# Performance work log

Measured on AMD Instinct MI355X. Metric: run time of the kernel, lower is better.

## Reference

```python
import jax, jax.numpy as jnp
import numpy as np

B, N, C = 4, 2048, 768
H = 12
HD = C // H  # 64


def setup_inputs() -> dict:
    key = jax.random.key(0)
    ks = jax.random.split(key, 6)
    s = 0.02
    return {
        "x": jax.random.normal(ks[0], (B, N, C), dtype=jnp.float32),
        "w_qkv": jax.random.normal(ks[1], (C, 3 * C), dtype=jnp.float32) * s,
        "b_qkv": jax.random.normal(ks[2], (3 * C,), dtype=jnp.float32) * s,
        "w_proj": jax.random.normal(ks[3], (C, C), dtype=jnp.float32) * s,
        "b_proj": jax.random.normal(ks[4], (C,), dtype=jnp.float32) * s,
        "key_log_bias": jax.random.normal(ks[5], (B, N), dtype=jnp.float32),
    }


def reference(x, w_qkv, b_qkv, w_proj, b_proj, key_log_bias):
    b, n, c = x.shape
    scale = 1.0 / float(HD) ** 0.5
    qkv = x @ w_qkv + b_qkv                      # [B, N, 3C]
    qkv = qkv.reshape(b, n, 3, H, HD).transpose(2, 0, 3, 1, 4)  # [3, B, H, N, HD]
    q, k, v = qkv[0], qkv[1], qkv[2]
    logits = jnp.einsum('bhqd,bhkd->bhqk', q, k) * scale        # [B, H, N, N]
    logits = logits + key_log_bias[:, None, None, :]            # key-side bias
    attn = jax.nn.softmax(logits, axis=-1)
    out = jnp.einsum('bhqk,bhkd->bhqd', attn, v)                # [B, H, N, HD]
    out = out.transpose(0, 2, 1, 3).reshape(b, n, c)            # [B, N, C]
    return out @ w_proj + b_proj
```

## Files before the change

### kernel.cpp

```cpp
#include <hip/hip_runtime.h>


typedef short short8 __attribute__((ext_vector_type(8)));
typedef float f32x4 __attribute__((ext_vector_type(4)));
typedef unsigned int u32x4 __attribute__((ext_vector_type(4)));

#define GLB_AS(p) ((const __attribute__((address_space(1))) void*)(p))
#define LDS_AS(p) ((__attribute__((address_space(3))) void*)(p))

__device__ __forceinline__ void gload_lds16(const void* g, void* l) {
  __builtin_amdgcn_global_load_lds(GLB_AS(g), LDS_AS(l), 16, 0, 0);
}

__device__ __forceinline__ f32x4 mfma16(short8 a, short8 b, f32x4 c) {
  return __builtin_amdgcn_mfma_f32_16x16x32_bf16(a, b, c, 0, 0, 0);
}

__device__ __forceinline__ unsigned short f2bf(float f) {
  union { float f; unsigned u; } v; v.f = f;
  unsigned r = v.u + 0x7fffu + ((v.u >> 16) & 1u);
  return (unsigned short)(r >> 16);
}

__device__ __forceinline__ unsigned cvt_pk_bf16(float a, float b) {
  unsigned r;
  asm("v_cvt_pk_bf16_f32 %0, %1, %2" : "=v"(r) : "v"(a), "v"(b));
  return r;
}

#define LOG2E 1.44269504088896340736f

__device__ __forceinline__ int kappa1(int m) {
  return ((m >> 4) & 1) * 32 + ((m >> 2) & 3) * 8 + ((m >> 5) & 1) * 4 + (m & 3);
}


__global__ __launch_bounds__(256) void cvt_f32_bf16(const float* __restrict__ in,
                                                    unsigned short* __restrict__ out,
                                                    int n8) {
  int i = blockIdx.x * 256 + threadIdx.x;
  if (i >= n8) return;
  const float4* p = (const float4*)in + 2 * (size_t)i;
  float4 a = p[0], c = p[1];
  short8 r;
  r[0] = (short)f2bf(a.x); r[1] = (short)f2bf(a.y); r[2] = (short)f2bf(a.z); r[3] = (short)f2bf(a.w);
  r[4] = (short)f2bf(c.x); r[5] = (short)f2bf(c.y); r[6] = (short)f2bf(c.z); r[7] = (short)f2bf(c.w);
  ((short8*)out)[i] = r;
}

__global__ __launch_bounds__(256) void scale_bias(const float* __restrict__ in,
                                                  float* __restrict__ out, int n) {
  int i = blockIdx.x * 256 + threadIdx.x;
  if (i >= n) return;
  int m = i & 63;
  out[i] = in[(i & ~63) + kappa1(m)] * LOG2E;
}

__global__ __launch_bounds__(256) void tr_cvt_f32_bf16(const float* __restrict__ src,
                                                       unsigned short* __restrict__ dst,
                                                       int R, int C) {
  __shared__ float t[32][33];
  int tx = threadIdx.x & 31, ty = threadIdx.x >> 5;
  int c0 = blockIdx.x * 32, r0 = blockIdx.y * 32;
#pragma unroll
  for (int i = 0; i < 32; i += 8)
    t[ty + i][tx] = src[(size_t)(r0 + ty + i) * C + c0 + tx];
  __syncthreads();
#pragma unroll
  for (int i = 0; i < 32; i += 8)
    dst[(size_t)(c0 + ty + i) * R + r0 + tx] = f2bf(t[tx][ty + i]);
}

__global__ __launch_bounds__(256) void tr_bf16_head(const unsigned short* __restrict__ src,
                                                    unsigned short* __restrict__ dst) {
  __shared__ unsigned short t[32][33];
  int tx = threadIdx.x & 31, ty = threadIdx.x >> 5;
  size_t hb = (size_t)blockIdx.z * (2048 * 64);
  int c0 = blockIdx.x * 32, r0 = blockIdx.y * 32;
#pragma unroll
  for (int i = 0; i < 32; i += 8)
    t[ty + i][tx] = src[hb + (size_t)(r0 + ty + i) * 64 + c0 + tx];
  __syncthreads();
#pragma unroll
  for (int i = 0; i < 32; i += 8)
    dst[hb + (size_t)(c0 + ty + i) * 2048 + r0 + tx] = t[tx][ty + i];
}

template <int EPI>
__global__ __launch_bounds__(256, 2) void gemm_bt(
    const unsigned short* __restrict__ A, const unsigned short* __restrict__ Bt,
    const float* __restrict__ bias, float* __restrict__ outf,
    unsigned short* __restrict__ qo, unsigned short* __restrict__ ko,
    unsigned short* __restrict__ vo, int K) {
  __shared__ __align__(16) unsigned short As[128 * 64];
  __shared__ __align__(16) unsigned short Bs[128 * 64];
  const int tid = threadIdx.x;
  const int lane = tid & 63, wid = tid >> 6;
  const int lr = lane & 15, lg = lane >> 4;
  const int bm = blockIdx.x, bn = blockIdx.y;
  const int wr = (wid >> 1) * 64, wc = (wid & 1) * 64;

  const unsigned short* ap[4];
  const unsigned short* bp[4];
  unsigned loff[4];
#pragma unroll
  for (int i = 0; i < 4; ++i) {
    int c = wid * 4 + i;
    int r = c * 8 + (lane >> 3);
    int gs = (lane & 7) ^ (r & 7);
    ap[i] = A + (size_t)(bm * 128 + r) * K + gs * 8;
    bp[i] = Bt + (size_t)(bn * 128 + r) * K + gs * 8;
    loff[i] = (unsigned)c * 1024;
  }

  f32x4 acc[4][4] = {};
  const int nt = K >> 6;
  for (int t = 0; t < nt; ++t) {
#pragma unroll
    for (int i = 0; i < 4; ++i) {
      gload_lds16(ap[i], (char*)As + loff[i]);
      gload_lds16(bp[i], (char*)Bs + loff[i]);
      ap[i] += 64;
      bp[i] += 64;
    }
    __syncthreads();
#pragma unroll
    for (int kkk = 0; kkk < 2; ++kkk) {
      short8 af[4], bf[4];
#pragma unroll
      for (int mf = 0; mf < 4; ++mf) {
        int r = wr + mf * 16 + lr;
        int g = kkk * 4 + lg;
        af[mf] = *(const short8*)((const char*)As + r * 128 + ((g ^ (r & 7)) << 4));
      }
#pragma unroll
      for (int nf = 0; nf < 4; ++nf) {
        int r = wc + nf * 16 + lr;
        int g = kkk * 4 + lg;
        bf[nf] = *(const short8*)((const char*)Bs + r * 128 + ((g ^ (r & 7)) << 4));
      }
#pragma unroll
      for (int mf = 0; mf < 4; ++mf)
#pragma unroll
        for (int nf = 0; nf < 4; ++nf)
          acc[mf][nf] = mfma16(af[mf], bf[nf], acc[mf][nf]);
    }
    __syncthreads();
  }

  const int colbase = bn * 128 + wc;
  float bv[4];
#pragma unroll
  for (int nf = 0; nf < 4; ++nf) bv[nf] = bias[colbase + nf * 16 + lr];

  if constexpr (EPI == 0) {
#pragma unroll
    for (int nf = 0; nf < 4; ++nf) {
      int col = colbase + nf * 16 + lr;
      int which = col / 768;
      int rem = col - which * 768;
      int h = rem >> 6, d = rem & 63;
#pragma unroll
      for (int mf = 0; mf < 4; ++mf) {
#pragma unroll
        for (int j = 0; j < 4; ++j) {
          int row = bm * 128 + wr + mf * 16 + lg * 4 + j;
          int bb = row >> 11, nn = row & 2047;
          float v = acc[mf][nf][j] + bv[nf];
          size_t off = (((size_t)bb * 12 + h) * 2048 + nn) * 64 + d;
          if (which == 0)
            qo[off] = f2bf(v * (0.125f * LOG2E));
          else if (which == 1)
            ko[off] = f2bf(v);
          else
            vo[off] = f2bf(v);
        }
      }
    }
  } else {
#pragma unroll
    for (int mf = 0; mf < 4; ++mf) {
#pragma unroll
      for (int j = 0; j < 4; ++j) {
        int row = bm * 128 + wr + mf * 16 + lg * 4 + j;
#pragma unroll
        for (int nf = 0; nf < 4; ++nf) {
          int col = colbase + nf * 16 + lr;
          outf[(size_t)row * 768 + col] = acc[mf][nf][j] + bv[nf];
        }
      }
    }
  }
}

__global__ __launch_bounds__(256, 3) void attn_fused(
    const unsigned short* __restrict__ Q, const unsigned short* __restrict__ Kx,
    const unsigned short* __restrict__ Vt, const float* __restrict__ klb,
    unsigned short* __restrict__ Ao) {
  __shared__ __align__(16) unsigned short Ks[64 * 64];
  __shared__ __align__(16) unsigned short Vs[64 * 64];
  const int tid = threadIdx.x, lane = tid & 63, wid = tid >> 6;
  const int lr = lane & 15, lg = lane >> 4;
  const int qb = blockIdx.x, bh = blockIdx.y;
  const int b = bh / 12, h = bh - b * 12;
  const size_t hoff = (size_t)bh * (2048 * 64);
  const unsigned short* Qh = Q + hoff;
  const unsigned short* Kh = Kx + hoff;
  const unsigned short* Vh = Vt + hoff;
  const float* kb = klb + b * 2048;

  short8 qf[2][2];
#pragma unroll
  for (int mf = 0; mf < 2; ++mf)
#pragma unroll
    for (int kkk = 0; kkk < 2; ++kkk) {
      int qr = qb * 128 + wid * 32 + mf * 16 + lr;
      qf[mf][kkk] = *(const short8*)(Qh + (size_t)qr * 64 + kkk * 32 + lg * 8);
    }

  const int c0 = wid * 2, c1 = wid * 2 + 1;
  const int r0s = c0 * 8 + (lane >> 3), r1s = c1 * 8 + (lane >> 3);
  const int g0 = (lane & 7) ^ (r0s & 7), g1 = (lane & 7) ^ (r1s & 7);
  const int k1r0 = kappa1(r0s), k1r1 = kappa1(r1s);

  f32x4 o[2][4] = {};
  f32x4 ol[2] = {};

  short8 ones;
#pragma unroll
  for (int e = 0; e < 8; ++e) ones[e] = (short)0x3F80;

  for (int t = 0; t < 32; ++t) {
    const int kt0 = t * 64;
    gload_lds16(Kh + (size_t)(kt0 + k1r0) * 64 + g0 * 8, (char*)Ks + c0 * 1024);
    gload_lds16(Kh + (size_t)(kt0 + k1r1) * 64 + g1 * 8, (char*)Ks + c1 * 1024);
    gload_lds16(Vh + (size_t)r0s * 2048 + kt0 + g0 * 8, (char*)Vs + c0 * 1024);
    gload_lds16(Vh + (size_t)r1s * 2048 + kt0 + g1 * 8, (char*)Vs + c1 * 1024);
    __syncthreads();

    f32x4 bias4[4];
#pragma unroll
    for (int nf = 0; nf < 4; ++nf)
      bias4[nf] = *(const f32x4*)(kb + kt0 + nf * 16 + lg * 4);

    f32x4 s[4][2] = {};
#pragma unroll
    for (int kkk = 0; kkk < 2; ++kkk) {
      short8 kf[4];
#pragma unroll
      for (int nf = 0; nf < 4; ++nf) {
        int r = nf * 16 + lr, g = kkk * 4 + lg;
        kf[nf] = *(const short8*)((const char*)Ks + r * 128 + ((g ^ (r & 7)) << 4));
      }
#pragma unroll
      for (int nf = 0; nf < 4; ++nf)
#pragma unroll
        for (int mf = 0; mf < 2; ++mf)
          s[nf][mf] = mfma16(kf[nf], qf[mf][kkk], s[nf][mf]);
    }

#pragma unroll
    for (int nf = 0; nf < 4; ++nf)
#pragma unroll
      for (int mf = 0; mf < 2; ++mf)
#pragma unroll
        for (int j = 0; j < 4; ++j)
          s[nf][mf][j] = __builtin_exp2f(s[nf][mf][j] + bias4[nf][j]);

    short8 pa[2][2];
#pragma unroll
    for (int mf = 0; mf < 2; ++mf)
#pragma unroll
      for (int kkk = 0; kkk < 2; ++kkk) {
        u32x4 w;
        w[0] = cvt_pk_bf16(s[kkk][mf][0], s[kkk][mf][1]);
        w[1] = cvt_pk_bf16(s[kkk][mf][2], s[kkk][mf][3]);
        w[2] = cvt_pk_bf16(s[kkk + 2][mf][0], s[kkk + 2][mf][1]);
        w[3] = cvt_pk_bf16(s[kkk + 2][mf][2], s[kkk + 2][mf][3]);
        pa[mf][kkk] = __builtin_bit_cast(short8, w);
      }

#pragma unroll
    for (int kkk = 0; kkk < 2; ++kkk) {
      short8 vf[4];
#pragma unroll
      for (int nf = 0; nf < 4; ++nf) {
        int r = nf * 16 + lr, g = kkk * 4 + lg;
        vf[nf] = *(const short8*)((const char*)Vs + r * 128 + ((g ^ (r & 7)) << 4));
      }
#pragma unroll
      for (int mf = 0; mf < 2; ++mf) {
        ol[mf] = mfma16(pa[mf][kkk], ones, ol[mf]);
#pragma unroll
        for (int nf = 0; nf < 4; ++nf)
          o[mf][nf] = mfma16(pa[mf][kkk], vf[nf], o[mf][nf]);
      }
    }
    __syncthreads();
  }

#pragma unroll
  for (int mf = 0; mf < 2; ++mf)
#pragma unroll
    for (int j = 0; j < 4; ++j) {
      float inv = 1.f / ol[mf][j];
      int qr = qb * 128 + wid * 32 + mf * 16 + lg * 4 + j;
#pragma unroll
      for (int nf = 0; nf < 4; ++nf) {
        int d = nf * 16 + lr;
        Ao[((size_t)b * 2048 + qr) * 768 + h * 64 + d] = f2bf(o[mf][nf][j] * inv);
      }
    }
}


extern "C" void kernel_launch(void* const* d_in, const int* in_sizes, int n_in,
                              void* d_out, int out_size, void* d_ws, size_t ws_size,
                              hipStream_t stream) {
  (void)in_sizes; (void)n_in; (void)out_size; (void)ws_size;
  const float* x = (const float*)d_in[0];
  const float* wqkv = (const float*)d_in[1];
  const float* bqkv = (const float*)d_in[2];
  const float* wproj = (const float*)d_in[3];
  const float* bproj = (const float*)d_in[4];
  const float* klb = (const float*)d_in[5];
  float* out = (float*)d_out;
  char* ws = (char*)d_ws;

  const size_t SZ = (size_t)8192 * 768 * 2;
  unsigned short* xb = (unsigned short*)(ws);
  unsigned short* wqkvT = (unsigned short*)(ws + SZ);
  unsigned short* wprojT = (unsigned short*)(ws + SZ + 3538944);
  unsigned short* qbuf = (unsigned short*)(ws + SZ + 3538944 + 1179648);
  unsigned short* kbuf = (unsigned short*)(ws + SZ + 3538944 + 1179648 + SZ);
  unsigned short* vbuf = (unsigned short*)(ws + SZ + 3538944 + 1179648 + 2 * SZ);
  unsigned short* vtbuf = (unsigned short*)(ws + SZ + 3538944 + 1179648 + 3 * SZ);
  float* klbs = (float*)(ws + SZ + 3538944 + 1179648 + 4 * SZ);
  unsigned short* aob = xb;

  cvt_f32_bf16<<<dim3(3072), dim3(256), 0, stream>>>(x, xb, 786432);
  scale_bias<<<dim3(32), dim3(256), 0, stream>>>(klb, klbs, 8192);
  tr_cvt_f32_bf16<<<dim3(72, 24), dim3(256), 0, stream>>>(wqkv, wqkvT, 768, 2304);
  tr_cvt_f32_bf16<<<dim3(24, 24), dim3(256), 0, stream>>>(wproj, wprojT, 768, 768);
  gemm_bt<0><<<dim3(64, 18), dim3(256), 0, stream>>>(xb, wqkvT, bqkv, nullptr,
                                                     qbuf, kbuf, vbuf, 768);
  tr_bf16_head<<<dim3(2, 64, 48), dim3(256), 0, stream>>>(vbuf, vtbuf);
  attn_fused<<<dim3(16, 48), dim3(256), 0, stream>>>(qbuf, kbuf, vtbuf, klbs, aob);
  gemm_bt<1><<<dim3(64, 6), dim3(256), 0, stream>>>(aob, wprojT, bproj, out,
                                                    nullptr, nullptr, nullptr, 768);
}
```

Measured before the change: 166.2 us.

## Fold exp(key bias) into V and row-sum weights; double-buffer K/V tiles

Result: faster. 158.5 us (-4.6%).

```diff
diff --git a/kernel.cpp b/kernel.cpp
--- a/kernel.cpp
+++ b/kernel.cpp
@@ -20,6 +20,11 @@
   union { float f; unsigned u; } v; v.f = f;
   unsigned r = v.u + 0x7fffu + ((v.u >> 16) & 1u);
   return (unsigned short)(r >> 16);
+}
+
+__device__ __forceinline__ float bf2f(unsigned short u) {
+  union { unsigned u; float f; } v; v.u = ((unsigned)u) << 16;
+  return v.f;
 }
 
 __device__ __forceinline__ unsigned cvt_pk_bf16(float a, float b) {
@@ -48,12 +53,10 @@
   ((short8*)out)[i] = r;
 }
 
-__global__ __launch_bounds__(256) void scale_bias(const float* __restrict__ in,
-                                                  float* __restrict__ out, int n) {
+__global__ __launch_bounds__(256) void exp_bias(const float* __restrict__ in,
+                                                unsigned short* __restrict__ out, int n) {
   int i = blockIdx.x * 256 + threadIdx.x;
-  if (i >= n) return;
-  int m = i & 63;
-  out[i] = in[(i & ~63) + kappa1(m)] * LOG2E;
+  if (i < n) out[i] = f2bf(__builtin_exp2f(in[i] * LOG2E));
 }
 
 __global__ __launch_bounds__(256) void tr_cvt_f32_bf16(const float* __restrict__ src,
@@ -72,18 +75,21 @@
 }
 
 __global__ __launch_bounds__(256) void tr_bf16_head(const unsigned short* __restrict__ src,
+                                                    const unsigned short* __restrict__ ebb,
                                                     unsigned short* __restrict__ dst) {
   __shared__ unsigned short t[32][33];
   int tx = threadIdx.x & 31, ty = threadIdx.x >> 5;
   size_t hb = (size_t)blockIdx.z * (2048 * 64);
+  int b = blockIdx.z / 12;
   int c0 = blockIdx.x * 32, r0 = blockIdx.y * 32;
 #pragma unroll
   for (int i = 0; i < 32; i += 8)
     t[ty + i][tx] = src[hb + (size_t)(r0 + ty + i) * 64 + c0 + tx];
   __syncthreads();
+  float eb = bf2f(ebb[b * 2048 + r0 + tx]);
 #pragma unroll
   for (int i = 0; i < 32; i += 8)
-    dst[hb + (size_t)(c0 + ty + i) * 2048 + r0 + tx] = t[tx][ty + i];
+    dst[hb + (size_t)(c0 + ty + i) * 2048 + r0 + tx] = f2bf(bf2f(t[tx][ty + i]) * eb);
 }
 
 template <int EPI>
@@ -195,10 +201,10 @@
 
 __global__ __launch_bounds__(256, 3) void attn_fused(
     const unsigned short* __restrict__ Q, const unsigned short* __restrict__ Kx,
-    const unsigned short* __restrict__ Vt, const float* __restrict__ klb,
+    const unsigned short* __restrict__ Vt, const unsigned short* __restrict__ ebb,
     unsigned short* __restrict__ Ao) {
-  __shared__ __align__(16) unsigned short Ks[64 * 64];
-  __shared__ __align__(16) unsigned short Vs[64 * 64];
+  __shared__ __align__(16) unsigned short Ks[2][64 * 64];
+  __shared__ __align__(16) unsigned short Vs[2][64 * 64];
   const int tid = threadIdx.x, lane = tid & 63, wid = tid >> 6;
   const int lr = lane & 15, lg = lane >> 4;
   const int qb = blockIdx.x, bh = blockIdx.y;
@@ -207,7 +213,7 @@
   const unsigned short* Qh = Q + hoff;
   const unsigned short* Kh = Kx + hoff;
   const unsigned short* Vh = Vt + hoff;
-  const float* kb = klb + b * 2048;
+  const unsigned short* ebh = ebb + b * 2048;
 
   short8 qf[2][2];
 #pragma unroll
@@ -226,22 +232,28 @@
   f32x4 o[2][4] = {};
   f32x4 ol[2] = {};
 
-  short8 ones;
-#pragma unroll
-  for (int e = 0; e < 8; ++e) ones[e] = (short)0x3F80;
+#define STAGE(buf, t)                                                                  \
+  do {                                                                                 \
+    const int kt0_ = (t) * 64;                                                         \
+    gload_lds16(Kh + (size_t)(kt0_ + k1r0) * 64 + g0 * 8, (char*)Ks[buf] + c0 * 1024); \
+    gload_lds16(Kh + (size_t)(kt0_ + k1r1) * 64 + g1 * 8, (char*)Ks[buf] + c1 * 1024); \
+    gload_lds16(Vh + (size_t)r0s * 2048 + kt0_ + g0 * 8, (char*)Vs[buf] + c0 * 1024);  \
+    gload_lds16(Vh + (size_t)r1s * 2048 + kt0_ + g1 * 8, (char*)Vs[buf] + c1 * 1024);  \
+  } while (0)
+
+  STAGE(0, 0);
+  int cur = 0;
 
   for (int t = 0; t < 32; ++t) {
+    __syncthreads();
+    if (t + 1 < 32) STAGE(cur ^ 1, t + 1);
+
     const int kt0 = t * 64;
-    gload_lds16(Kh + (size_t)(kt0 + k1r0) * 64 + g0 * 8, (char*)Ks + c0 * 1024);
-    gload_lds16(Kh + (size_t)(kt0 + k1r1) * 64 + g1 * 8, (char*)Ks + c1 * 1024);
-    gload_lds16(Vh + (size_t)r0s * 2048 + kt0 + g0 * 8, (char*)Vs + c0 * 1024);
-    gload_lds16(Vh + (size_t)r1s * 2048 + kt0 + g1 * 8, (char*)Vs + c1 * 1024);
-    __syncthreads();
-
-    f32x4 bias4[4];
-#pragma unroll
-    for (int nf = 0; nf < 4; ++nf)
-      bias4[nf] = *(const f32x4*)(kb + kt0 + nf * 16 + lg * 4);
+
+    short8 ebf[2];
+#pragma unroll
+    for (int kkk = 0; kkk < 2; ++kkk)
+      ebf[kkk] = *(const short8*)(ebh + kt0 + kkk * 32 + lg * 8);
 
     f32x4 s[4][2] = {};
 #pragma unroll
@@ -250,7 +262,7 @@
 #pragma unroll
       for (int nf = 0; nf < 4; ++nf) {
         int r = nf * 16 + lr, g = kkk * 4 + lg;
-        kf[nf] = *(const short8*)((const char*)Ks + r * 128 + ((g ^ (r & 7)) << 4));
+        kf[nf] = *(const short8*)((const char*)Ks[cur] + r * 128 + ((g ^ (r & 7)) << 4));
       }
 #pragma unroll
       for (int nf = 0; nf < 4; ++nf)
@@ -265,7 +277,7 @@
       for (int mf = 0; mf < 2; ++mf)
 #pragma unroll
         for (int j = 0; j < 4; ++j)
-          s[nf][mf][j] = __builtin_exp2f(s[nf][mf][j] + bias4[nf][j]);
+          s[nf][mf][j] = __builtin_exp2f(s[nf][mf][j]);
 
     short8 pa[2][2];
 #pragma unroll
@@ -286,18 +298,19 @@
 #pragma unroll
       for (int nf = 0; nf < 4; ++nf) {
         int r = nf * 16 + lr, g = kkk * 4 + lg;
-        vf[nf] = *(const short8*)((const char*)Vs + r * 128 + ((g ^ (r & 7)) << 4));
+        vf[nf] = *(const short8*)((const char*)Vs[cur] + r * 128 + ((g ^ (r & 7)) << 4));
       }
 #pragma unroll
       for (int mf = 0; mf < 2; ++mf) {
-        ol[mf] = mfma16(pa[mf][kkk], ones, ol[mf]);
+        ol[mf] = mfma16(pa[mf][kkk], ebf[kkk], ol[mf]);
 #pragma unroll
         for (int nf = 0; nf < 4; ++nf)
           o[mf][nf] = mfma16(pa[mf][kkk], vf[nf], o[mf][nf]);
       }
     }
-    __syncthreads();
+    cur ^= 1;
   }
+#undef STAGE
 
 #pragma unroll
   for (int mf = 0; mf < 2; ++mf)
@@ -335,17 +348,17 @@
   unsigned short* kbuf = (unsigned short*)(ws + SZ + 3538944 + 1179648 + SZ);
   unsigned short* vbuf = (unsigned short*)(ws + SZ + 3538944 + 1179648 + 2 * SZ);
   unsigned short* vtbuf = (unsigned short*)(ws + SZ + 3538944 + 1179648 + 3 * SZ);
-  float* klbs = (float*)(ws + SZ + 3538944 + 1179648 + 4 * SZ);
+  unsigned short* ebb = (unsigned short*)(ws + SZ + 3538944 + 1179648 + 4 * SZ);
   unsigned short* aob = xb;
 
   cvt_f32_bf16<<<dim3(3072), dim3(256), 0, stream>>>(x, xb, 786432);
-  scale_bias<<<dim3(32), dim3(256), 0, stream>>>(klb, klbs, 8192);
+  exp_bias<<<dim3(32), dim3(256), 0, stream>>>(klb, ebb, 8192);
   tr_cvt_f32_bf16<<<dim3(72, 24), dim3(256), 0, stream>>>(wqkv, wqkvT, 768, 2304);
   tr_cvt_f32_bf16<<<dim3(24, 24), dim3(256), 0, stream>>>(wproj, wprojT, 768, 768);
   gemm_bt<0><<<dim3(64, 18), dim3(256), 0, stream>>>(xb, wqkvT, bqkv, nullptr,
                                                      qbuf, kbuf, vbuf, 768);
-  tr_bf16_head<<<dim3(2, 64, 48), dim3(256), 0, stream>>>(vbuf, vtbuf);
-  attn_fused<<<dim3(16, 48), dim3(256), 0, stream>>>(qbuf, kbuf, vtbuf, klbs, aob);
+  tr_bf16_head<<<dim3(2, 64, 48), dim3(256), 0, stream>>>(vbuf, ebb, vtbuf);
+  attn_fused<<<dim3(16, 48), dim3(256), 0, stream>>>(qbuf, kbuf, vtbuf, ebb, aob);
   gemm_bt<1><<<dim3(64, 6), dim3(256), 0, stream>>>(aob, wprojT, bproj, out,
                                                     nullptr, nullptr, nullptr, 768);
 }
```
